# Kernel optimization log

Hardware: AMD Instinct MI355X
Metric: run time of the kernel (lower is better)

The kernel has to match this reference:

```python
import jax, jax.numpy as jnp
import numpy as np

BATCH = 16384
NUM_IN = 4096
NUM_OUT = 1024
NNZ = 262144
BN_EPS = 1e-3  # keras BatchNormalization default epsilon


def setup_inputs() -> dict:
    key = jax.random.key(0)
    ks = jax.random.split(key, 6)
    x = jax.random.normal(ks[0], (BATCH, NUM_IN), dtype=jnp.float32)
    sp_values = jax.random.normal(ks[1], (NNZ,), dtype=jnp.float32)
    gamma = jnp.ones((NUM_IN,), dtype=jnp.float32)
    beta = jnp.zeros((NUM_IN,), dtype=jnp.float32)
    moving_mean = jax.random.normal(ks[2], (NUM_IN,), dtype=jnp.float32)
    # positive moving variance in [0.5, 1.5)
    moving_var = jax.random.uniform(ks[3], (NUM_IN,), dtype=jnp.float32, minval=0.5, maxval=1.5)
    sp_rows = jax.random.randint(ks[4], (NNZ,), 0, NUM_IN, dtype=jnp.int32)
    sp_cols = jax.random.randint(ks[5], (NNZ,), 0, NUM_OUT, dtype=jnp.int32)
    return {
        "x": x,
        "sp_values": sp_values,
        "gamma": gamma,
        "beta": beta,
        "moving_mean": moving_mean,
        "moving_var": moving_var,
        "sp_rows": sp_rows,
        "sp_cols": sp_cols,
    }


def reference(x, sp_values, gamma, beta, moving_mean, moving_var, sp_rows, sp_cols):
    # BatchNorm (inference mode, moving statistics), fused elementwise
    h = (x - moving_mean) * (gamma * jax.lax.rsqrt(moving_var + BN_EPS)) + beta
    # Scatter the fixed-index sparse weights into a small dense [NUM_IN, NUM_OUT]
    # matrix (16 MB), then a single dense GEMM — honors SparseTensor semantics
    # (duplicate indices accumulate) while staying GEMM-efficient.
    W = jnp.zeros((NUM_IN, NUM_OUT), dtype=x.dtype).at[sp_rows, sp_cols].add(sp_values)
    return h @ W  # [BATCH, NUM_OUT]
```

## Files before the change

### kernel.cpp

```cpp
#include <hip/hip_runtime.h>
#include <hip/hip_bf16.h>

#define BATCH   16384
#define NUM_IN  4096
#define NUM_OUT 1024
#define NNZ     262144
#define BN_EPS  1e-3f

typedef __attribute__((ext_vector_type(8)))  short short8;
typedef __attribute__((ext_vector_type(4)))  float f32x4;
typedef __attribute__((ext_vector_type(4)))  unsigned int u32x4;

typedef __attribute__((address_space(3))) void        lds_void_t;
typedef const __attribute__((address_space(1))) void  g_void_t;

__device__ inline unsigned short f2bf(float f) {
    unsigned int u = __builtin_bit_cast(unsigned int, f);
    u += 0x7fffu + ((u >> 16) & 1u);
    return (unsigned short)(u >> 16);
}

__global__ void k_zero(f32x4* __restrict__ p) {
    p[(size_t)blockIdx.x * 256 + threadIdx.x] = f32x4{0.f, 0.f, 0.f, 0.f};
}

__global__ void k_scatter(const float* __restrict__ v, const int* __restrict__ r,
                          const int* __restrict__ c, float* __restrict__ wtf) {
    int i = blockIdx.x * 256 + threadIdx.x;
    atomicAdd(&wtf[(size_t)c[i] * NUM_IN + r[i]], v[i]);
}

__global__ void k_wprep(const float* __restrict__ wtf, const float* __restrict__ gamma,
                        const float* __restrict__ beta, const float* __restrict__ mean,
                        const float* __restrict__ var, unsigned short* __restrict__ wtb,
                        float* __restrict__ bias) {
    const int n = blockIdx.x;
    const int t = threadIdx.x;
    float acc = 0.f;
    for (int k = t; k < NUM_IN; k += 256) {
        float w = wtf[(size_t)n * NUM_IN + k];
        float s = gamma[k] * rsqrtf(var[k] + BN_EPS);
        wtb[(size_t)n * NUM_IN + k] = f2bf(w * s);
        acc += (beta[k] - mean[k] * s) * w;
    }
    #pragma unroll
    for (int o = 32; o; o >>= 1) acc += __shfl_down(acc, o, 64);
    __shared__ float red[4];
    if ((t & 63) == 0) red[t >> 6] = acc;
    __syncthreads();
    if (t == 0) bias[n] = red[0] + red[1] + red[2] + red[3];
}

#define BM 256
#define BN 256
#define BK 32
#define NT (NUM_IN / BK)
#define ASLOT 32768
#define BSLOT 16384
#define PSLOT 49152

__global__ __launch_bounds__(512, 2) void k_gemm(const float* __restrict__ x,
                                                 const unsigned short* __restrict__ wt,
                                                 const float* __restrict__ bias,
                                                 float* __restrict__ out) {
    __shared__ __align__(128) char lds[3 * PSLOT];

    const int bid = blockIdx.x;
    const int swz = (bid & 7) * 32 + (bid >> 3);
    const int m0 = (swz >> 2) * BM;
    const int n0 = (swz & 3) * BN;

    const int t    = threadIdx.x;
    const int lane = t & 63;
    const int wid  = t >> 6;
    const int wm   = wid >> 2;
    const int wn   = wid & 3;

    const char* xb = (const char*)x;
    const char* wb = (const char*)wt;

    auto stageA = [&](int kt, int sl) {
        #pragma unroll
        for (int i = 0; i < 4; ++i) {
            int row = i * 64 + (t >> 3);
            size_t src = (size_t)(m0 + row) * (NUM_IN * 4) + (size_t)kt * (BK * 4)
                       + (((t & 7) ^ (row & 7)) * 16);
            __builtin_amdgcn_global_load_lds((g_void_t*)(xb + src),
                (lds_void_t*)(lds + sl * PSLOT + i * 8192 + t * 16), 16, 0, 0);
        }
    };
    auto stageB = [&](int kt, int sl) {
        #pragma unroll
        for (int i = 0; i < 2; ++i) {
            int row = i * 128 + (t >> 2);
            size_t src = (size_t)(n0 + row) * (NUM_IN * 2) + (size_t)kt * (BK * 2)
                       + (((t & 3) ^ ((row >> 1) & 3)) * 16);
            __builtin_amdgcn_global_load_lds((g_void_t*)(wb + src),
                (lds_void_t*)(lds + sl * PSLOT + ASLOT + i * 8192 + t * 16), 16, 0, 0);
        }
    };

    const int fr   = lane & 15;
    const int a_k0 = (lane >> 4) * 32;
    const int b_k0 = (lane >> 4) * 16;

    f32x4 alo[4], ahi[4];
    short8 af[4], bfr[4];

    auto readB4 = [&](const char* B) {
        #pragma unroll
        for (int n = 0; n < 4; ++n) {
            int row = wn * 64 + n * 16 + fr;
            bfr[n] = *(const short8*)(B + row * 64 + (b_k0 ^ (((row >> 1) & 3) << 4)));
        }
    };
    auto readA4 = [&](const char* A, int mh) {
        #pragma unroll
        for (int m = 0; m < 4; ++m) {
            int row = wm * 128 + (mh + m) * 16 + fr;
            int s = (row & 7) << 4;
            alo[m] = *(const f32x4*)(A + row * 128 + (a_k0 ^ s));
            ahi[m] = *(const f32x4*)(A + row * 128 + ((a_k0 + 16) ^ s));
        }
    };
    auto convA = [&]() {
        #pragma unroll
        for (int m = 0; m < 4; ++m) {
            const unsigned int* f0 = (const unsigned int*)&alo[m];
            const unsigned int* f1 = (const unsigned int*)&ahi[m];
            u32x4 p;
            p[0] = __builtin_amdgcn_perm(f0[1], f0[0], 0x07060302u);
            p[1] = __builtin_amdgcn_perm(f0[3], f0[2], 0x07060302u);
            p[2] = __builtin_amdgcn_perm(f1[1], f1[0], 0x07060302u);
            p[3] = __builtin_amdgcn_perm(f1[3], f1[2], 0x07060302u);
            af[m] = __builtin_bit_cast(short8, p);
        }
    };

    f32x4 acc[8][4] = {};
    auto mfma16 = [&](int mh) {
        __builtin_amdgcn_s_setprio(1);
        #pragma unroll
        for (int m = 0; m < 4; ++m)
            #pragma unroll
            for (int n = 0; n < 4; ++n)
                acc[mh + m][n] = __builtin_amdgcn_mfma_f32_16x16x32_bf16(
                    af[m], bfr[n], acc[mh + m][n], 0, 0, 0);
        __builtin_amdgcn_s_setprio(0);
    };

    stageA(0, 0); stageB(0, 0);
    stageA(1, 1); stageB(1, 1);
    asm volatile("s_waitcnt vmcnt(6)" ::: "memory");
    __builtin_amdgcn_s_barrier();

    int cur = 0;
    #pragma unroll 1
    for (int kt = 0; kt < NT; ++kt) {
        const bool st = (kt + 2) < NT;
        const int stg = (cur >= 1) ? cur - 1 : cur + 2;
        const char* A = lds + cur * PSLOT;
        const char* B = A + ASLOT;
        if (st) stageA(kt + 2, stg);
        readB4(B);
        readA4(A, 0);
        __builtin_amdgcn_s_barrier();
        asm volatile("s_waitcnt lgkmcnt(0)" ::: "memory");
        __builtin_amdgcn_sched_barrier(0);
        convA();
        mfma16(0);
        __builtin_amdgcn_s_barrier();
        if (st) stageB(kt + 2, stg);
        readA4(A, 4);
        if (st) asm volatile("s_waitcnt vmcnt(6)" ::: "memory");
        else    asm volatile("s_waitcnt vmcnt(0)" ::: "memory");
        __builtin_amdgcn_s_barrier();
        asm volatile("s_waitcnt lgkmcnt(0)" ::: "memory");
        __builtin_amdgcn_sched_barrier(0);
        convA();
        mfma16(4);
        __builtin_amdgcn_s_barrier();
        cur = (cur < 2) ? cur + 1 : 0;
    }

    float bj[4];
    #pragma unroll
    for (int n = 0; n < 4; ++n) bj[n] = bias[n0 + wn * 64 + n * 16 + fr];
    const int mb = m0 + wm * 128 + (lane >> 4) * 4;
    const int nb = n0 + wn * 64 + fr;
    #pragma unroll
    for (int m = 0; m < 8; ++m)
        #pragma unroll
        for (int n = 0; n < 4; ++n)
            #pragma unroll
            for (int r = 0; r < 4; ++r)
                out[(size_t)(mb + m * 16 + r) * NUM_OUT + (nb + n * 16)] =
                    acc[m][n][r] + bj[n];
}

extern "C" void kernel_launch(void* const* d_in, const int* in_sizes, int n_in,
                              void* d_out, int out_size, void* d_ws, size_t ws_size,
                              hipStream_t stream) {
    const float* x     = (const float*)d_in[0];
    const float* spv   = (const float*)d_in[1];
    const float* gamma = (const float*)d_in[2];
    const float* beta  = (const float*)d_in[3];
    const float* mean  = (const float*)d_in[4];
    const float* var   = (const float*)d_in[5];
    const int*   rows  = (const int*)d_in[6];
    const int*   cols  = (const int*)d_in[7];
    float* out = (float*)d_out;

    float* wtf = (float*)d_out;
    unsigned short* wtb = (unsigned short*)d_ws;
    float* bias = (float*)((char*)d_ws + (size_t)NUM_IN * NUM_OUT * sizeof(unsigned short));

    hipLaunchKernelGGL(k_zero, dim3((NUM_IN * NUM_OUT / 4) / 256), dim3(256), 0, stream,
                       (f32x4*)wtf);
    hipLaunchKernelGGL(k_scatter, dim3(NNZ / 256), dim3(256), 0, stream,
                       spv, rows, cols, wtf);
    hipLaunchKernelGGL(k_wprep, dim3(NUM_OUT), dim3(256), 0, stream,
                       wtf, gamma, beta, mean, var, wtb, bias);
    hipLaunchKernelGGL(k_gemm, dim3((BATCH / BM) * (NUM_OUT / BN)), dim3(512), 0, stream,
                       x, wtb, bias, out);
}
```

Baseline: 206.3 us.

## Restructure GEMM wave tiling to 64x128 and store operands in fragment-native LDS layout

The wave grid changes from 2x4 to 4x2, so each wave owns a 64x128 output tile. A fragments are converted to bf16 once per k-step instead of twice, while B is split into two halves. The global-to-LDS staging now writes data already in MFMA fragment order, so each lane reads its fragment with a contiguous lane*16 access and the XOR swizzle goes away. The per-iteration barrier count drops from four to two. The risks are less coalesced global loads, since each thread's source addresses are now spread across rows, and a possible race because the trailing barrier that protected slot reuse has been removed.

New measurement: 239.2 us. 1.16x slower.

```diff
diff --git a/kernel.cpp b/kernel.cpp
--- a/kernel.cpp
+++ b/kernel.cpp
@@ -55,9 +55,8 @@
 #define BN 256
 #define BK 32
 #define NT (NUM_IN / BK)
-#define ASLOT 32768
-#define BSLOT 16384
 #define PSLOT 49152
+#define BOFF 32768
 
 __global__ __launch_bounds__(512, 2) void k_gemm(const float* __restrict__ x,
                                                  const unsigned short* __restrict__ wt,
@@ -73,8 +72,8 @@
     const int t    = threadIdx.x;
     const int lane = t & 63;
     const int wid  = t >> 6;
-    const int wm   = wid >> 2;
-    const int wn   = wid & 3;
+    const int wm   = wid >> 1;
+    const int wn   = wid & 1;
 
     const char* xb = (const char*)x;
     const char* wb = (const char*)wt;
@@ -82,9 +81,9 @@
     auto stageA = [&](int kt, int sl) {
         #pragma unroll
         for (int i = 0; i < 4; ++i) {
-            int row = i * 64 + (t >> 3);
-            size_t src = (size_t)(m0 + row) * (NUM_IN * 4) + (size_t)kt * (BK * 4)
-                       + (((t & 7) ^ (row & 7)) * 16);
+            int row = m0 + ((i & 1) * 8 + (t >> 6)) * 16 + (t & 15);
+            size_t src = (size_t)row * (NUM_IN * 4) + (size_t)kt * (BK * 4)
+                       + ((t >> 4) & 3) * 32 + (i >> 1) * 16;
             __builtin_amdgcn_global_load_lds((g_void_t*)(xb + src),
                 (lds_void_t*)(lds + sl * PSLOT + i * 8192 + t * 16), 16, 0, 0);
         }
@@ -92,37 +91,18 @@
     auto stageB = [&](int kt, int sl) {
         #pragma unroll
         for (int i = 0; i < 2; ++i) {
-            int row = i * 128 + (t >> 2);
-            size_t src = (size_t)(n0 + row) * (NUM_IN * 2) + (size_t)kt * (BK * 2)
-                       + (((t & 3) ^ ((row >> 1) & 3)) * 16);
+            int col = n0 + (i * 8 + (t >> 6)) * 16 + (t & 15);
+            size_t src = (size_t)col * (NUM_IN * 2) + (size_t)kt * (BK * 2)
+                       + ((t >> 4) & 3) * 16;
             __builtin_amdgcn_global_load_lds((g_void_t*)(wb + src),
-                (lds_void_t*)(lds + sl * PSLOT + ASLOT + i * 8192 + t * 16), 16, 0, 0);
+                (lds_void_t*)(lds + sl * PSLOT + BOFF + i * 8192 + t * 16), 16, 0, 0);
         }
     };
 
-    const int fr   = lane & 15;
-    const int a_k0 = (lane >> 4) * 32;
-    const int b_k0 = (lane >> 4) * 16;
-
     f32x4 alo[4], ahi[4];
-    short8 af[4], bfr[4];
-
-    auto readB4 = [&](const char* B) {
-        #pragma unroll
-        for (int n = 0; n < 4; ++n) {
-            int row = wn * 64 + n * 16 + fr;
-            bfr[n] = *(const short8*)(B + row * 64 + (b_k0 ^ (((row >> 1) & 3) << 4)));
-        }
-    };
-    auto readA4 = [&](const char* A, int mh) {
-        #pragma unroll
-        for (int m = 0; m < 4; ++m) {
-            int row = wm * 128 + (mh + m) * 16 + fr;
-            int s = (row & 7) << 4;
-            alo[m] = *(const f32x4*)(A + row * 128 + (a_k0 ^ s));
-            ahi[m] = *(const f32x4*)(A + row * 128 + ((a_k0 + 16) ^ s));
-        }
-    };
+    short8 af[4], bf0[4], bf1[4];
+    f32x4 acc[4][8] = {};
+
     auto convA = [&]() {
         #pragma unroll
         for (int m = 0; m < 4; ++m) {
@@ -137,61 +117,68 @@
         }
     };
 
-    f32x4 acc[8][4] = {};
-    auto mfma16 = [&](int mh) {
-        __builtin_amdgcn_s_setprio(1);
-        #pragma unroll
-        for (int m = 0; m < 4; ++m)
-            #pragma unroll
-            for (int n = 0; n < 4; ++n)
-                acc[mh + m][n] = __builtin_amdgcn_mfma_f32_16x16x32_bf16(
-                    af[m], bfr[n], acc[mh + m][n], 0, 0, 0);
-        __builtin_amdgcn_s_setprio(0);
-    };
-
     stageA(0, 0); stageB(0, 0);
     stageA(1, 1); stageB(1, 1);
     asm volatile("s_waitcnt vmcnt(6)" ::: "memory");
     __builtin_amdgcn_s_barrier();
 
-    int cur = 0;
+    int cur = 0, s2 = 2;
     #pragma unroll 1
     for (int kt = 0; kt < NT; ++kt) {
         const bool st = (kt + 2) < NT;
-        const int stg = (cur >= 1) ? cur - 1 : cur + 2;
-        const char* A = lds + cur * PSLOT;
-        const char* B = A + ASLOT;
-        if (st) stageA(kt + 2, stg);
-        readB4(B);
-        readA4(A, 0);
+        const char* A = lds + cur * PSLOT + (wm * 4) * 1024 + lane * 16;
+        const char* B = lds + cur * PSLOT + BOFF + (wn * 8) * 1024 + lane * 16;
+        if (st) stageA(kt + 2, s2);
+        #pragma unroll
+        for (int m = 0; m < 4; ++m) {
+            alo[m] = *(const f32x4*)(A + m * 1024);
+            ahi[m] = *(const f32x4*)(A + m * 1024 + 16384);
+        }
+        #pragma unroll
+        for (int n = 0; n < 4; ++n)
+            bf0[n] = *(const short8*)(B + n * 1024);
         __builtin_amdgcn_s_barrier();
         asm volatile("s_waitcnt lgkmcnt(0)" ::: "memory");
         __builtin_amdgcn_sched_barrier(0);
         convA();
-        mfma16(0);
-        __builtin_amdgcn_s_barrier();
-        if (st) stageB(kt + 2, stg);
-        readA4(A, 4);
-        if (st) asm volatile("s_waitcnt vmcnt(6)" ::: "memory");
-        else    asm volatile("s_waitcnt vmcnt(0)" ::: "memory");
+        __builtin_amdgcn_s_setprio(1);
+        #pragma unroll
+        for (int m = 0; m < 4; ++m)
+            #pragma unroll
+            for (int n = 0; n < 4; ++n)
+                acc[m][n] = __builtin_amdgcn_mfma_f32_16x16x32_bf16(
+                    af[m], bf0[n], acc[m][n], 0, 0, 0);
+        __builtin_amdgcn_s_setprio(0);
+        if (st) stageB(kt + 2, s2);
+        #pragma unroll
+        for (int n = 0; n < 4; ++n)
+            bf1[n] = *(const short8*)(B + (4 + n) * 1024);
+        if (st)                asm volatile("s_waitcnt vmcnt(6)" ::: "memory");
+        else if (kt + 1 < NT)  asm volatile("s_waitcnt vmcnt(0)" ::: "memory");
         __builtin_amdgcn_s_barrier();
         asm volatile("s_waitcnt lgkmcnt(0)" ::: "memory");
         __builtin_amdgcn_sched_barrier(0);
-        convA();
-        mfma16(4);
-        __builtin_amdgcn_s_barrier();
+        __builtin_amdgcn_s_setprio(1);
+        #pragma unroll
+        for (int m = 0; m < 4; ++m)
+            #pragma unroll
+            for (int n = 0; n < 4; ++n)
+                acc[m][n + 4] = __builtin_amdgcn_mfma_f32_16x16x32_bf16(
+                    af[m], bf1[n], acc[m][n + 4], 0, 0, 0);
+        __builtin_amdgcn_s_setprio(0);
         cur = (cur < 2) ? cur + 1 : 0;
+        s2  = (s2 < 2) ? s2 + 1 : 0;
     }
 
-    float bj[4];
+    float bj[8];
     #pragma unroll
-    for (int n = 0; n < 4; ++n) bj[n] = bias[n0 + wn * 64 + n * 16 + fr];
-    const int mb = m0 + wm * 128 + (lane >> 4) * 4;
-    const int nb = n0 + wn * 64 + fr;
+    for (int n = 0; n < 8; ++n) bj[n] = bias[n0 + wn * 128 + n * 16 + (lane & 15)];
+    const int mb = m0 + wm * 64 + (lane >> 4) * 4;
+    const int nb = n0 + wn * 128 + (lane & 15);
     #pragma unroll
-    for (int m = 0; m < 8; ++m)
-        #pragma unroll
-        for (int n = 0; n < 4; ++n)
+    for (int m = 0; m < 4; ++m)
+        #pragma unroll
+        for (int n = 0; n < 8; ++n)
             #pragma unroll
             for (int r = 0; r < 4; ++r)
                 out[(size_t)(mb + m * 16 + r) * NUM_OUT + (nb + n * 16)] =
```

## Convert A to bf16 once in registers and store bf16 tiles with BK=64

Applied to the files above, without the earlier changes.

The fp32 A tile is now loaded from global memory into registers, converted to bf16 once, and written to LDS in a fragment-friendly layout. Previously fp32 went to LDS directly and every wave repeated the conversion after each LDS read. BK doubles to 64 with a two-slot double buffer, and the K-step is split into four MFMA phases. This cuts LDS footprint per element and removes duplicated conversion work. The cost is more register pressure from holding 8 fp32 vectors, plus the global-to-LDS copy of A is no longer asynchronous.

New measurement: 218.1 us. +5.7%, slower.

```diff
diff --git a/kernel.cpp b/kernel.cpp
--- a/kernel.cpp
+++ b/kernel.cpp
@@ -9,7 +9,7 @@
 
 typedef __attribute__((ext_vector_type(8)))  short short8;
 typedef __attribute__((ext_vector_type(4)))  float f32x4;
-typedef __attribute__((ext_vector_type(4)))  unsigned int u32x4;
+typedef __attribute__((ext_vector_type(2)))  unsigned int u32x2;
 
 typedef __attribute__((address_space(3))) void        lds_void_t;
 typedef const __attribute__((address_space(1))) void  g_void_t;
@@ -53,17 +53,16 @@
 
 #define BM 256
 #define BN 256
-#define BK 32
+#define BK 64
 #define NT (NUM_IN / BK)
-#define ASLOT 32768
-#define BSLOT 16384
-#define PSLOT 49152
+#define SLOT 65536
+#define BOFF 32768
 
 __global__ __launch_bounds__(512, 2) void k_gemm(const float* __restrict__ x,
                                                  const unsigned short* __restrict__ wt,
                                                  const float* __restrict__ bias,
                                                  float* __restrict__ out) {
-    __shared__ __align__(128) char lds[3 * PSLOT];
+    __shared__ __align__(128) char lds[2 * SLOT];
 
     const int bid = blockIdx.x;
     const int swz = (bid & 7) * 32 + (bid >> 3);
@@ -79,123 +78,136 @@
     const char* xb = (const char*)x;
     const char* wb = (const char*)wt;
 
-    auto stageA = [&](int kt, int sl) {
+    const int cpo   = ((((lane & 15) << 2) | (lane >> 4)) * 16);
+    const int aRdW  = wm * 8192;
+    const int bColB = (wn * 64 + (lane & 15)) * 128;
+    const int bC0   = (((lane >> 4)    ) ^ (lane & 7)) * 16;
+    const int bC1   = ((4 + (lane >> 4)) ^ (lane & 7)) * 16;
+    const int awBase = ((t >> 3) & 1) * 16384 + (t >> 8) * 1024
+                     + ((((t >> 4) & 15) * 4 + ((t >> 1) & 3)) * 16) + (t & 1) * 8;
+
+    f32x4 rA[8];
+    auto loadA = [&](int kt) {
+        #pragma unroll
+        for (int i = 0; i < 8; ++i)
+            rA[i] = *(const f32x4*)(xb
+                + (size_t)(m0 + i * 32 + (t >> 4)) * (NUM_IN * 4)
+                + (size_t)kt * (BK * 4) + (t & 15) * 16);
+    };
+    auto convWriteA = [&](int sl) {
+        char* dst = lds + sl * SLOT + awBase;
+        #pragma unroll
+        for (int i = 0; i < 8; ++i) {
+            const unsigned int* f = (const unsigned int*)&rA[i];
+            u32x2 w;
+            w.x = __builtin_amdgcn_perm(f[1], f[0], 0x07060302u);
+            w.y = __builtin_amdgcn_perm(f[3], f[2], 0x07060302u);
+            *(u32x2*)(dst + i * 2048) = w;
+        }
+    };
+    auto stageB = [&](int kt, int sl) {
         #pragma unroll
         for (int i = 0; i < 4; ++i) {
-            int row = i * 64 + (t >> 3);
-            size_t src = (size_t)(m0 + row) * (NUM_IN * 4) + (size_t)kt * (BK * 4)
-                       + (((t & 7) ^ (row & 7)) * 16);
-            __builtin_amdgcn_global_load_lds((g_void_t*)(xb + src),
-                (lds_void_t*)(lds + sl * PSLOT + i * 8192 + t * 16), 16, 0, 0);
+            int col = i * 64 + (t >> 3);
+            size_t src = (size_t)(n0 + col) * (NUM_IN * 2) + (size_t)kt * (BK * 2)
+                       + (((t & 7) ^ ((t >> 3) & 7)) * 16);
+            __builtin_amdgcn_global_load_lds((g_void_t*)(wb + src),
+                (lds_void_t*)(lds + sl * SLOT + BOFF + i * 8192 + t * 16), 16, 0, 0);
         }
     };
-    auto stageB = [&](int kt, int sl) {
-        #pragma unroll
-        for (int i = 0; i < 2; ++i) {
-            int row = i * 128 + (t >> 2);
-            size_t src = (size_t)(n0 + row) * (NUM_IN * 2) + (size_t)kt * (BK * 2)
-                       + (((t & 3) ^ ((row >> 1) & 3)) * 16);
-            __builtin_amdgcn_global_load_lds((g_void_t*)(wb + src),
-                (lds_void_t*)(lds + sl * PSLOT + ASLOT + i * 8192 + t * 16), 16, 0, 0);
-        }
-    };
-
-    const int fr   = lane & 15;
-    const int a_k0 = (lane >> 4) * 32;
-    const int b_k0 = (lane >> 4) * 16;
-
-    f32x4 alo[4], ahi[4];
-    short8 af[4], bfr[4];
-
-    auto readB4 = [&](const char* B) {
-        #pragma unroll
-        for (int n = 0; n < 4; ++n) {
-            int row = wn * 64 + n * 16 + fr;
-            bfr[n] = *(const short8*)(B + row * 64 + (b_k0 ^ (((row >> 1) & 3) << 4)));
-        }
-    };
-    auto readA4 = [&](const char* A, int mh) {
-        #pragma unroll
-        for (int m = 0; m < 4; ++m) {
-            int row = wm * 128 + (mh + m) * 16 + fr;
-            int s = (row & 7) << 4;
-            alo[m] = *(const f32x4*)(A + row * 128 + (a_k0 ^ s));
-            ahi[m] = *(const f32x4*)(A + row * 128 + ((a_k0 + 16) ^ s));
-        }
-    };
-    auto convA = [&]() {
-        #pragma unroll
-        for (int m = 0; m < 4; ++m) {
-            const unsigned int* f0 = (const unsigned int*)&alo[m];
-            const unsigned int* f1 = (const unsigned int*)&ahi[m];
-            u32x4 p;
-            p[0] = __builtin_amdgcn_perm(f0[1], f0[0], 0x07060302u);
-            p[1] = __builtin_amdgcn_perm(f0[3], f0[2], 0x07060302u);
-            p[2] = __builtin_amdgcn_perm(f1[1], f1[0], 0x07060302u);
-            p[3] = __builtin_amdgcn_perm(f1[3], f1[2], 0x07060302u);
-            af[m] = __builtin_bit_cast(short8, p);
-        }
+
+    short8 af[4], bf0[4], bf1[4];
+    auto readA4 = [&](const char* A, int h, int mh) {
+        const char* base = A + h * 16384 + aRdW + mh * 4096 + cpo;
+        af[0] = *(const short8*)(base);
+        af[1] = *(const short8*)(base + 1024);
+        af[2] = *(const short8*)(base + 2048);
+        af[3] = *(const short8*)(base + 3072);
+    };
+    auto readB4 = [&](const char* B, int co, short8* bf) {
+        const char* base = B + bColB + co;
+        bf[0] = *(const short8*)(base);
+        bf[1] = *(const short8*)(base + 2048);
+        bf[2] = *(const short8*)(base + 4096);
+        bf[3] = *(const short8*)(base + 6144);
     };
 
     f32x4 acc[8][4] = {};
-    auto mfma16 = [&](int mh) {
+    auto mfma16 = [&](short8* bf, int mlb) {
         __builtin_amdgcn_s_setprio(1);
         #pragma unroll
-        for (int m = 0; m < 4; ++m)
+        for (int mi = 0; mi < 4; ++mi)
             #pragma unroll
-            for (int n = 0; n < 4; ++n)
-                acc[mh + m][n] = __builtin_amdgcn_mfma_f32_16x16x32_bf16(
-                    af[m], bfr[n], acc[mh + m][n], 0, 0, 0);
+            for (int nf = 0; nf < 4; ++nf)
+                acc[mlb + mi][nf] = __builtin_amdgcn_mfma_f32_16x16x32_bf16(
+                    af[mi], bf[nf], acc[mlb + mi][nf], 0, 0, 0);
         __builtin_amdgcn_s_setprio(0);
     };
 
-    stageA(0, 0); stageB(0, 0);
-    stageA(1, 1); stageB(1, 1);
-    asm volatile("s_waitcnt vmcnt(6)" ::: "memory");
+    loadA(0);
+    stageB(0, 0);
+    stageB(1, 1);
+    asm volatile("s_waitcnt vmcnt(8)" ::: "memory");
+    convWriteA(0);
+    asm volatile("s_waitcnt vmcnt(4)" ::: "memory");
+    asm volatile("s_waitcnt lgkmcnt(0)" ::: "memory");
     __builtin_amdgcn_s_barrier();
 
-    int cur = 0;
     #pragma unroll 1
     for (int kt = 0; kt < NT; ++kt) {
-        const bool st = (kt + 2) < NT;
-        const int stg = (cur >= 1) ? cur - 1 : cur + 2;
-        const char* A = lds + cur * PSLOT;
-        const char* B = A + ASLOT;
-        if (st) stageA(kt + 2, stg);
-        readB4(B);
-        readA4(A, 0);
-        __builtin_amdgcn_s_barrier();
-        asm volatile("s_waitcnt lgkmcnt(0)" ::: "memory");
-        __builtin_amdgcn_sched_barrier(0);
-        convA();
-        mfma16(0);
-        __builtin_amdgcn_s_barrier();
-        if (st) stageB(kt + 2, stg);
-        readA4(A, 4);
-        if (st) asm volatile("s_waitcnt vmcnt(6)" ::: "memory");
-        else    asm volatile("s_waitcnt vmcnt(0)" ::: "memory");
-        __builtin_amdgcn_s_barrier();
-        asm volatile("s_waitcnt lgkmcnt(0)" ::: "memory");
-        __builtin_amdgcn_sched_barrier(0);
-        convA();
-        mfma16(4);
-        __builtin_amdgcn_s_barrier();
-        cur = (cur < 2) ? cur + 1 : 0;
+        const int s = kt & 1;
+        const char* Ap = lds + s * SLOT;
+        const char* Bp = Ap + BOFF;
+        const bool st1 = (kt + 1) < NT;
+        const bool st2 = (kt + 2) < NT;
+        if (st1) loadA(kt + 1);
+        readB4(Bp, bC0, bf0);
+        readA4(Ap, 0, 0);
+        __builtin_amdgcn_s_barrier();
+        asm volatile("s_waitcnt lgkmcnt(0)" ::: "memory");
+        __builtin_amdgcn_sched_barrier(0);
+        mfma16(bf0, 0);
+        __builtin_amdgcn_s_barrier();
+        readA4(Ap, 0, 1);
+        __builtin_amdgcn_s_barrier();
+        asm volatile("s_waitcnt lgkmcnt(0)" ::: "memory");
+        __builtin_amdgcn_sched_barrier(0);
+        mfma16(bf0, 4);
+        __builtin_amdgcn_s_barrier();
+        readB4(Bp, bC1, bf1);
+        readA4(Ap, 1, 0);
+        __builtin_amdgcn_s_barrier();
+        asm volatile("s_waitcnt lgkmcnt(0)" ::: "memory");
+        __builtin_amdgcn_sched_barrier(0);
+        mfma16(bf1, 0);
+        __builtin_amdgcn_s_barrier();
+        if (st2) stageB(kt + 2, s);
+        readA4(Ap, 1, 1);
+        if (st1) {
+            if (st2) asm volatile("s_waitcnt vmcnt(4)" ::: "memory");
+            else     asm volatile("s_waitcnt vmcnt(0)" ::: "memory");
+            convWriteA(s ^ 1);
+        }
+        __builtin_amdgcn_s_barrier();
+        asm volatile("s_waitcnt lgkmcnt(0)" ::: "memory");
+        __builtin_amdgcn_sched_barrier(0);
+        mfma16(bf1, 4);
+        __builtin_amdgcn_s_barrier();
     }
 
     float bj[4];
     #pragma unroll
-    for (int n = 0; n < 4; ++n) bj[n] = bias[n0 + wn * 64 + n * 16 + fr];
+    for (int n = 0; n < 4; ++n) bj[n] = bias[n0 + wn * 64 + n * 16 + (lane & 15)];
     const int mb = m0 + wm * 128 + (lane >> 4) * 4;
-    const int nb = n0 + wn * 64 + fr;
+    const int nb = n0 + wn * 64 + (lane & 15);
     #pragma unroll
-    for (int m = 0; m < 8; ++m)
+    for (int ml = 0; ml < 8; ++ml)
         #pragma unroll
         for (int n = 0; n < 4; ++n)
             #pragma unroll
             for (int r = 0; r < 4; ++r)
-                out[(size_t)(mb + m * 16 + r) * NUM_OUT + (nb + n * 16)] =
-                    acc[m][n][r] + bj[n];
+                out[(size_t)(mb + ml * 16 + r) * NUM_OUT + (nb + n * 16)] =
+                    acc[ml][n][r] + bj[n];
 }
 
 extern "C" void kernel_launch(void* const* d_in, const int* in_sizes, int n_in,
```
